# Kernel tuning notes

Hardware: AMD Instinct MI355X
Metric: run time of the kernel (lower is better)

## Reference

```python
import jax, jax.numpy as jnp
import numpy as np


def _up2(x):
    return jnp.repeat(jnp.repeat(x, 2, axis=2), 2, axis=3)


def setup_inputs() -> dict:
    key = jax.random.key(0)
    ks = jax.random.split(key, 6)
    Vps, C, H, W = 32, 128, 64, 64
    return {
        "x1": jax.random.normal(ks[0], (Vps, C, H, W), dtype=jnp.float32),
        "x2": jax.random.normal(ks[1], (Vps, C, H // 2, W // 2), dtype=jnp.float32),
        "x3": jax.random.normal(ks[2], (Vps, C, H // 4, W // 4), dtype=jnp.float32),
        "x4": jax.random.normal(ks[3], (Vps, C, H // 4, W // 4), dtype=jnp.float32),
        "conv_w": jax.random.normal(ks[4], (128, 512), dtype=jnp.float32) * 0.02,
        "conv_b": jnp.zeros((128,), dtype=jnp.float32),
        "gamma": jnp.zeros((1,), dtype=jnp.float32),
        "weight": jnp.ones((128,), dtype=jnp.float32),
        "lin_w": jax.random.normal(ks[5], (1, 128), dtype=jnp.float32) * 0.1,
    }


def reference(x1, x2, x3, x4, conv_w, conv_b, gamma, weight, lin_w):
    # upsample lower pyramid levels to x1 resolution and concat on channels
    x_sm = jnp.concatenate([x1, _up2(x2), _up2(_up2(x3)), _up2(_up2(x4))], axis=1)
    # 1x1 conv: [Vps,512,H,W] x [128,512] -> [Vps,128,H,W]
    x_sm = jnp.einsum('vchw,oc->vohw', x_sm, conv_w) + conv_b[None, :, None, None]
    Vps, C, H, W = x_sm.shape

    # --- batch (viewport) attention ---
    gap = jnp.mean(x_sm, axis=(2, 3))                     # [Vps, C]
    v_q = gap @ lin_w.T                                    # [Vps, 1]
    att = v_q @ v_q.T                                      # [Vps, Vps]
    att_new = jnp.broadcast_to(jnp.max(att, axis=-1, keepdims=True), att.shape)
    vps_mat = jax.nn.softmax(att_new, axis=-1)             # rows constant -> uniform
    v_v = x_sm.reshape(Vps, C * H * W)
    vps_att = (vps_mat @ v_v).reshape(Vps, C, H, W)
    x_sm = vps_att * gamma + x_sm

    # --- channel attention ---
    c_q = jnp.mean(x_sm, axis=(2, 3))                      # [Vps, C]
    att_C = c_q.T @ c_q                                    # [C, C]
    C_mat = jax.nn.softmax(att_C, axis=-1) * weight        # broadcast over last dim
    c_v = x_sm.reshape(C, Vps * H * W)                     # faithful raw reshape as in torch
    C_att = (C_mat @ c_v).reshape(Vps, C, H, W)
    out = C_att + x_sm
    return out.reshape(Vps, C, H * W)
```

## Files before the change

### kernel.cpp

```cpp
#include <hip/hip_runtime.h>

#define V 32
#define CH 128
#define SP 4096

typedef __attribute__((ext_vector_type(8))) short bf16x8;
typedef __attribute__((ext_vector_type(4))) float f32x4;

__device__ __forceinline__ unsigned short bf16rne(float x) {
    union { float f; unsigned u; } v; v.f = x;
    unsigned r = v.u + 0x7fff + ((v.u >> 16) & 1);
    return (unsigned short)(r >> 16);
}

__device__ __forceinline__ int xswz(int s) { return (s & 7) ^ ((s >> 2) & 7); }

__device__ __forceinline__ const float* xsm_row(const float* xsm, int j, int r) {
    return xsm + ((size_t)((j >> 2) * CH + (j & 3) * 32 + r)) * SP;
}

__global__ __launch_bounds__(256) void prep_w(const float* __restrict__ W,
                                              unsigned short* __restrict__ Wpad)
{
    int row = blockIdx.x;
    int j = threadIdx.x;
    if (j < 136) {
        int sigma = row >> 7, o = row & 127;
        float v = (j < 128) ? W[o * 512 + sigma * 128 + j] : 0.f;
        Wpad[row * 136 + j] = bf16rne(v);
    }
}

__global__ __launch_bounds__(256) void conv_lo(
    const float* __restrict__ xa, const float* __restrict__ xb,
    const unsigned short* __restrict__ WA, const unsigned short* __restrict__ WB,
    int spatial, int nph, float* __restrict__ outbuf)
{
    __shared__ __align__(16) unsigned short Wl[128 * 136];
    __shared__ __align__(16) unsigned short Xl[64 * 128];
    const int v = blockIdx.y, sc = blockIdx.x, tid = threadIdx.x;
    const int lane = tid & 63, w = tid >> 6;
    const int l15 = lane & 15, quad = lane >> 4;
    const int o0 = (w >> 1) * 64, s0 = (w & 1) * 32;
    const int sq = tid & 15, cp0 = tid >> 4;

    f32x4 acc[4][2];
#pragma unroll
    for (int it = 0; it < 4; ++it)
#pragma unroll
        for (int st = 0; st < 2; ++st) acc[it][st] = (f32x4){0.f, 0.f, 0.f, 0.f};

#pragma unroll 1
    for (int ph = 0; ph < nph; ++ph) {
        if (ph) __syncthreads();
        const float* xp = ph ? xb : xa;
        const unsigned short* wp = ph ? WB : WA;
        {
            const float4* wsrc = (const float4*)wp;
            float4* wdst = (float4*)Wl;
            for (int idx = tid; idx < 2176; idx += 256) wdst[idx] = wsrc[idx];
        }
        const float* xbase = xp + (size_t)v * CH * spatial + sc * 64;
#pragma unroll
        for (int rep = 0; rep < 4; ++rep) {
            int c = (cp0 + rep * 16) * 2;
            const float* r0 = xbase + (size_t)c * spatial + sq * 4;
            float4 va = *(const float4*)r0;
            float4 vb = *(const float4*)(r0 + spatial);
            float a4[4] = {va.x, va.y, va.z, va.w};
            float b4[4] = {vb.x, vb.y, vb.z, vb.w};
#pragma unroll
            for (int i = 0; i < 4; ++i) {
                int s = sq * 4 + i;
                ushort2 pk; pk.x = bf16rne(a4[i]); pk.y = bf16rne(b4[i]);
                *(ushort2*)&Xl[s * 128 + (((c >> 3) ^ xswz(s)) * 8) + (c & 7)] = pk;
            }
        }
        __syncthreads();
#pragma unroll
        for (int ks = 0; ks < 4; ++ks) {
            int kb = ks * 4 + quad;
            bf16x8 af[4], bfr[2];
#pragma unroll
            for (int it = 0; it < 4; ++it)
                af[it] = *(const bf16x8*)&Wl[(o0 + it * 16 + l15) * 136 + ks * 32 + quad * 8];
#pragma unroll
            for (int st = 0; st < 2; ++st) {
                int s = s0 + st * 16 + l15;
                bfr[st] = *(const bf16x8*)&Xl[s * 128 + ((kb ^ xswz(s)) * 8)];
            }
#pragma unroll
            for (int it = 0; it < 4; ++it)
#pragma unroll
                for (int st = 0; st < 2; ++st)
                    acc[it][st] = __builtin_amdgcn_mfma_f32_16x16x32_bf16(
                        af[it], bfr[st], acc[it][st], 0, 0, 0);
        }
    }
#pragma unroll
    for (int it = 0; it < 4; ++it)
#pragma unroll
        for (int reg = 0; reg < 4; ++reg) {
            int o = o0 + it * 16 + quad * 4 + reg;
            float* orow = outbuf + ((size_t)(v * CH + o)) * spatial + sc * 64;
#pragma unroll
            for (int st = 0; st < 2; ++st) {
                int s_l = s0 + st * 16 + l15;
                orow[s_l] = acc[it][st][reg];
            }
        }
}

__global__ __launch_bounds__(256) void conv_full(
    const float* __restrict__ x1, const unsigned short* __restrict__ W0,
    const float* __restrict__ bias, const float* __restrict__ conv2,
    const float* __restrict__ conv34, float* __restrict__ xsm,
    float* __restrict__ gap)
{
    __shared__ __align__(16) unsigned short Wl[128 * 136];
    __shared__ __align__(16) unsigned short Xl[64 * 128];
    __shared__ float gscr[4][64];
    const int v = blockIdx.y, sc = blockIdx.x, tid = threadIdx.x;
    const int lane = tid & 63, w = tid >> 6;
    const int l15 = lane & 15, quad = lane >> 4;
    const int o0 = (w >> 1) * 64, s0 = (w & 1) * 32;
    const int sq = tid & 15, cp0 = tid >> 4;

    f32x4 acc[4][2];
#pragma unroll
    for (int it = 0; it < 4; ++it)
#pragma unroll
        for (int st = 0; st < 2; ++st) acc[it][st] = (f32x4){0.f, 0.f, 0.f, 0.f};

    {
        const float4* wsrc = (const float4*)W0;
        float4* wdst = (float4*)Wl;
        for (int idx = tid; idx < 2176; idx += 256) wdst[idx] = wsrc[idx];
    }
    const float* xbase = x1 + (size_t)v * CH * SP + sc * 64;
#pragma unroll
    for (int rep = 0; rep < 4; ++rep) {
        int c = (cp0 + rep * 16) * 2;
        const float* r0 = xbase + (size_t)c * SP + sq * 4;
        float4 va = *(const float4*)r0;
        float4 vb = *(const float4*)(r0 + SP);
        float a4[4] = {va.x, va.y, va.z, va.w};
        float b4[4] = {vb.x, vb.y, vb.z, vb.w};
#pragma unroll
        for (int i = 0; i < 4; ++i) {
            int s = sq * 4 + i;
            ushort2 pk; pk.x = bf16rne(a4[i]); pk.y = bf16rne(b4[i]);
            *(ushort2*)&Xl[s * 128 + (((c >> 3) ^ xswz(s)) * 8) + (c & 7)] = pk;
        }
    }
    __syncthreads();
#pragma unroll
    for (int ks = 0; ks < 4; ++ks) {
        int kb = ks * 4 + quad;
        bf16x8 af[4], bfr[2];
#pragma unroll
        for (int it = 0; it < 4; ++it)
            af[it] = *(const bf16x8*)&Wl[(o0 + it * 16 + l15) * 136 + ks * 32 + quad * 8];
#pragma unroll
        for (int st = 0; st < 2; ++st) {
            int s = s0 + st * 16 + l15;
            bfr[st] = *(const bf16x8*)&Xl[s * 128 + ((kb ^ xswz(s)) * 8)];
        }
#pragma unroll
        for (int it = 0; it < 4; ++it)
#pragma unroll
            for (int st = 0; st < 2; ++st)
                acc[it][st] = __builtin_amdgcn_mfma_f32_16x16x32_bf16(
                    af[it], bfr[st], acc[it][st], 0, 0, 0);
    }

    const float* c2row = conv2 + (size_t)v * CH * 1024 + (sc >> 1) * 32;
    const float* c34row = conv34 + (size_t)v * CH * 256 + (sc >> 2) * 16;
    float gs[16];
#pragma unroll
    for (int it = 0; it < 4; ++it)
#pragma unroll
        for (int reg = 0; reg < 4; ++reg) {
            int o = o0 + it * 16 + quad * 4 + reg;
            float b = bias[o];
            float* orow = xsm + ((size_t)(v * CH + o)) * SP + sc * 64;
            const float* c2p = c2row + (size_t)o * 1024;
            const float* c34p = c34row + (size_t)o * 256;
            float lsum = 0.f;
#pragma unroll
            for (int st = 0; st < 2; ++st) {
                int s_l = s0 + st * 16 + l15;
                float val = acc[it][st][reg] + b + c2p[s_l >> 1] + c34p[s_l >> 2];
                orow[s_l] = val;
                lsum += val;
            }
            gs[it * 4 + reg] = lsum;
        }
#pragma unroll
    for (int m = 1; m < 16; m <<= 1)
#pragma unroll
        for (int k = 0; k < 16; ++k) gs[k] += __shfl_xor(gs[k], m, 64);
    if (l15 == 0) {
#pragma unroll
        for (int it = 0; it < 4; ++it)
#pragma unroll
            for (int reg = 0; reg < 4; ++reg)
                gscr[w][it * 16 + quad * 4 + reg] = gs[it * 4 + reg];
    }
    __syncthreads();
    if (tid < 128) {
        int o = tid, b2 = (o >> 6) * 2;
        atomicAdd(&gap[v * CH + o], gscr[b2][o & 63] + gscr[b2 + 1][o & 63]);
    }
}

__global__ __launch_bounds__(128) void build_G(
    const float* __restrict__ gap, const float* __restrict__ gammap,
    const float* __restrict__ weight, unsigned short* __restrict__ GsPad)
{
    __shared__ float cq[32][128];
    __shared__ float red[128];
    const int i = blockIdx.x, j = threadIdx.x;
    const float g = gammap[0];

    float gb = 0.f;
    for (int v = 0; v < 32; ++v) gb += gap[v * CH + j];
    gb = gb * (1.f / 32.f) * (1.f / 4096.f) * g;
    for (int v = 0; v < 32; ++v) cq[v][j] = gap[v * CH + j] * (1.f / 4096.f) + gb;
    __syncthreads();

    float a = 0.f;
    for (int v = 0; v < 32; ++v) a += cq[v][i] * cq[v][j];

    red[j] = a; __syncthreads();
    float m = -1e30f;
    for (int t = 0; t < 128; ++t) m = fmaxf(m, red[t]);
    __syncthreads();
    float e = __expf(a - m);
    red[j] = e; __syncthreads();
    float ssum = 0.f;
    for (int t = 0; t < 128; ++t) ssum += red[t];
    float cm = e / ssum * weight[j] + ((i == j) ? 1.f : 0.f);
    __syncthreads();
    red[j] = cm; __syncthreads();
    float rs = 0.f;
    for (int t = (j & 3); t < 128; t += 4) rs += red[t];
    float gfull = cm + g * (1.f / 32.f) * rs;
    GsPad[i * 136 + j] = bf16rne(gfull - ((i == j) ? 1.f : 0.f));
}

__global__ __launch_bounds__(256) void apply_G(
    float* __restrict__ xsm, const unsigned short* __restrict__ GsPad)
{
    __shared__ __align__(16) unsigned short Gl[128 * 136];
    __shared__ __align__(16) unsigned short Xl[64 * 128];
    const int r = blockIdx.y, sc = blockIdx.x, tid = threadIdx.x;
    const int lane = tid & 63, w = tid >> 6;
    const int l15 = lane & 15, quad = lane >> 4;
    const int i0 = (w >> 1) * 64, s0 = (w & 1) * 32;
    const int sq = tid & 15, cp0 = tid >> 4;

    f32x4 acc[4][2];
#pragma unroll
    for (int it = 0; it < 4; ++it)
#pragma unroll
        for (int st = 0; st < 2; ++st) acc[it][st] = (f32x4){0.f, 0.f, 0.f, 0.f};

    {
        const float4* gsrc = (const float4*)GsPad;
        float4* gdst = (float4*)Gl;
        for (int idx = tid; idx < 2176; idx += 256) gdst[idx] = gsrc[idx];
    }
#pragma unroll
    for (int rep = 0; rep < 4; ++rep) {
        int c = (cp0 + rep * 16) * 2;
        const float* r0 = xsm_row(xsm, c, r) + sc * 64 + sq * 4;
        const float* r1 = xsm_row(xsm, c + 1, r) + sc * 64 + sq * 4;
        float4 va = *(const float4*)r0;
        float4 vb = *(const float4*)r1;
        float a4[4] = {va.x, va.y, va.z, va.w};
        float b4[4] = {vb.x, vb.y, vb.z, vb.w};
#pragma unroll
        for (int i = 0; i < 4; ++i) {
            int s = sq * 4 + i;
            ushort2 pk; pk.x = bf16rne(a4[i]); pk.y = bf16rne(b4[i]);
            *(ushort2*)&Xl[s * 128 + (((c >> 3) ^ xswz(s)) * 8) + (c & 7)] = pk;
        }
    }
    __syncthreads();
#pragma unroll
    for (int ks = 0; ks < 4; ++ks) {
        int kb = ks * 4 + quad;
        bf16x8 af[4], bfr[2];
#pragma unroll
        for (int it = 0; it < 4; ++it)
            af[it] = *(const bf16x8*)&Gl[(i0 + it * 16 + l15) * 136 + ks * 32 + quad * 8];
#pragma unroll
        for (int st = 0; st < 2; ++st) {
            int s = s0 + st * 16 + l15;
            bfr[st] = *(const bf16x8*)&Xl[s * 128 + ((kb ^ xswz(s)) * 8)];
        }
#pragma unroll
        for (int it = 0; it < 4; ++it)
#pragma unroll
            for (int st = 0; st < 2; ++st)
                acc[it][st] = __builtin_amdgcn_mfma_f32_16x16x32_bf16(
                    af[it], bfr[st], acc[it][st], 0, 0, 0);
    }
#pragma unroll
    for (int it = 0; it < 4; ++it)
#pragma unroll
        for (int reg = 0; reg < 4; ++reg) {
            int i = i0 + it * 16 + quad * 4 + reg;
            float* rowp = (float*)xsm_row(xsm, i, r) + sc * 64;
#pragma unroll
            for (int st = 0; st < 2; ++st) {
                int s_l = s0 + st * 16 + l15;
                rowp[s_l] = rowp[s_l] + acc[it][st][reg];
            }
        }
}

extern "C" void kernel_launch(void* const* d_in, const int* in_sizes, int n_in,
                              void* d_out, int out_size, void* d_ws, size_t ws_size,
                              hipStream_t stream)
{
    const float* x1     = (const float*)d_in[0];
    const float* x2     = (const float*)d_in[1];
    const float* x3     = (const float*)d_in[2];
    const float* x4     = (const float*)d_in[3];
    const float* conv_w = (const float*)d_in[4];
    const float* conv_b = (const float*)d_in[5];
    const float* gamma  = (const float*)d_in[6];
    const float* weight = (const float*)d_in[7];

    float* out = (float*)d_out;
    float* ws  = (float*)d_ws;

    float* conv2  = ws;
    float* conv34 = ws + (size_t)4194304;
    float* gap    = ws + (size_t)5242880;
    unsigned short* Wpad  = (unsigned short*)(ws + (size_t)5246976);
    unsigned short* GsPad = (unsigned short*)(ws + (size_t)5281792);

    hipMemsetAsync(gap, 0, 4096 * sizeof(float), stream);

    prep_w<<<512, 256, 0, stream>>>(conv_w, Wpad);
    conv_lo<<<dim3(16, 32), 256, 0, stream>>>(x2, x2, Wpad + 1 * 128 * 136,
                                              Wpad + 1 * 128 * 136, 1024, 1, conv2);
    conv_lo<<<dim3(4, 32), 256, 0, stream>>>(x3, x4, Wpad + 2 * 128 * 136,
                                             Wpad + 3 * 128 * 136, 256, 2, conv34);
    conv_full<<<dim3(64, 32), 256, 0, stream>>>(x1, Wpad, conv_b, conv2, conv34, out, gap);
    build_G<<<128, 128, 0, stream>>>(gap, gamma, weight, GsPad);
    apply_G<<<dim3(64, 32), 256, 0, stream>>>(out, GsPad);
}
```

Measured before the change: 214.7 us.

## Fuse low-resolution convs into full conv via upsampled K-chunks

Removes the two conv_lo kernels and their intermediate buffers. conv_full now upsamples x2, x3 and x4 into shared memory, does the full K=512 reduction as four 128-wide MFMA chunks, and reads weights straight from global memory instead of staging them in LDS. apply_G likewise reads G directly from global memory. This saves kernel launches and the workspace round-trip, but conv_full does four times the MFMA work per block on upsampled data the old code computed once at low resolution, and weight reads now go uncached through global/L2.

Result: slower. 263.5 us (+22.7%).

```diff
diff --git a/kernel.cpp b/kernel.cpp
--- a/kernel.cpp
+++ b/kernel.cpp
@@ -19,112 +19,27 @@
     return xsm + ((size_t)((j >> 2) * CH + (j & 3) * 32 + r)) * SP;
 }
 
-__global__ __launch_bounds__(256) void prep_w(const float* __restrict__ W,
+__global__ __launch_bounds__(128) void prep_w(const float* __restrict__ W,
                                               unsigned short* __restrict__ Wpad)
 {
     int row = blockIdx.x;
     int j = threadIdx.x;
-    if (j < 136) {
-        int sigma = row >> 7, o = row & 127;
-        float v = (j < 128) ? W[o * 512 + sigma * 128 + j] : 0.f;
-        Wpad[row * 136 + j] = bf16rne(v);
-    }
-}
-
-__global__ __launch_bounds__(256) void conv_lo(
-    const float* __restrict__ xa, const float* __restrict__ xb,
-    const unsigned short* __restrict__ WA, const unsigned short* __restrict__ WB,
-    int spatial, int nph, float* __restrict__ outbuf)
-{
-    __shared__ __align__(16) unsigned short Wl[128 * 136];
-    __shared__ __align__(16) unsigned short Xl[64 * 128];
-    const int v = blockIdx.y, sc = blockIdx.x, tid = threadIdx.x;
-    const int lane = tid & 63, w = tid >> 6;
-    const int l15 = lane & 15, quad = lane >> 4;
-    const int o0 = (w >> 1) * 64, s0 = (w & 1) * 32;
-    const int sq = tid & 15, cp0 = tid >> 4;
-
-    f32x4 acc[4][2];
-#pragma unroll
-    for (int it = 0; it < 4; ++it)
-#pragma unroll
-        for (int st = 0; st < 2; ++st) acc[it][st] = (f32x4){0.f, 0.f, 0.f, 0.f};
-
-#pragma unroll 1
-    for (int ph = 0; ph < nph; ++ph) {
-        if (ph) __syncthreads();
-        const float* xp = ph ? xb : xa;
-        const unsigned short* wp = ph ? WB : WA;
-        {
-            const float4* wsrc = (const float4*)wp;
-            float4* wdst = (float4*)Wl;
-            for (int idx = tid; idx < 2176; idx += 256) wdst[idx] = wsrc[idx];
-        }
-        const float* xbase = xp + (size_t)v * CH * spatial + sc * 64;
-#pragma unroll
-        for (int rep = 0; rep < 4; ++rep) {
-            int c = (cp0 + rep * 16) * 2;
-            const float* r0 = xbase + (size_t)c * spatial + sq * 4;
-            float4 va = *(const float4*)r0;
-            float4 vb = *(const float4*)(r0 + spatial);
-            float a4[4] = {va.x, va.y, va.z, va.w};
-            float b4[4] = {vb.x, vb.y, vb.z, vb.w};
-#pragma unroll
-            for (int i = 0; i < 4; ++i) {
-                int s = sq * 4 + i;
-                ushort2 pk; pk.x = bf16rne(a4[i]); pk.y = bf16rne(b4[i]);
-                *(ushort2*)&Xl[s * 128 + (((c >> 3) ^ xswz(s)) * 8) + (c & 7)] = pk;
-            }
-        }
-        __syncthreads();
-#pragma unroll
-        for (int ks = 0; ks < 4; ++ks) {
-            int kb = ks * 4 + quad;
-            bf16x8 af[4], bfr[2];
-#pragma unroll
-            for (int it = 0; it < 4; ++it)
-                af[it] = *(const bf16x8*)&Wl[(o0 + it * 16 + l15) * 136 + ks * 32 + quad * 8];
-#pragma unroll
-            for (int st = 0; st < 2; ++st) {
-                int s = s0 + st * 16 + l15;
-                bfr[st] = *(const bf16x8*)&Xl[s * 128 + ((kb ^ xswz(s)) * 8)];
-            }
-#pragma unroll
-            for (int it = 0; it < 4; ++it)
-#pragma unroll
-                for (int st = 0; st < 2; ++st)
-                    acc[it][st] = __builtin_amdgcn_mfma_f32_16x16x32_bf16(
-                        af[it], bfr[st], acc[it][st], 0, 0, 0);
-        }
-    }
-#pragma unroll
-    for (int it = 0; it < 4; ++it)
-#pragma unroll
-        for (int reg = 0; reg < 4; ++reg) {
-            int o = o0 + it * 16 + quad * 4 + reg;
-            float* orow = outbuf + ((size_t)(v * CH + o)) * spatial + sc * 64;
-#pragma unroll
-            for (int st = 0; st < 2; ++st) {
-                int s_l = s0 + st * 16 + l15;
-                orow[s_l] = acc[it][st][reg];
-            }
-        }
+    int sigma = row >> 7, o = row & 127;
+    Wpad[row * 128 + j] = bf16rne(W[o * 512 + sigma * 128 + j]);
 }
 
 __global__ __launch_bounds__(256) void conv_full(
-    const float* __restrict__ x1, const unsigned short* __restrict__ W0,
-    const float* __restrict__ bias, const float* __restrict__ conv2,
-    const float* __restrict__ conv34, float* __restrict__ xsm,
-    float* __restrict__ gap)
-{
-    __shared__ __align__(16) unsigned short Wl[128 * 136];
+    const float* __restrict__ x1, const float* __restrict__ x2,
+    const float* __restrict__ x3, const float* __restrict__ x4,
+    const unsigned short* __restrict__ Wpad, const float* __restrict__ bias,
+    float* __restrict__ xsm, float* __restrict__ gap)
+{
     __shared__ __align__(16) unsigned short Xl[64 * 128];
     __shared__ float gscr[4][64];
     const int v = blockIdx.y, sc = blockIdx.x, tid = threadIdx.x;
     const int lane = tid & 63, w = tid >> 6;
     const int l15 = lane & 15, quad = lane >> 4;
     const int o0 = (w >> 1) * 64, s0 = (w & 1) * 32;
-    const int sq = tid & 15, cp0 = tid >> 4;
 
     f32x4 acc[4][2];
 #pragma unroll
@@ -132,50 +47,99 @@
 #pragma unroll
         for (int st = 0; st < 2; ++st) acc[it][st] = (f32x4){0.f, 0.f, 0.f, 0.f};
 
+    auto mfma_chunk = [&](const unsigned short* __restrict__ Wsl) {
+#pragma unroll
+        for (int ks = 0; ks < 4; ++ks) {
+            int kb = ks * 4 + quad;
+            bf16x8 af[4], bfr[2];
+#pragma unroll
+            for (int it = 0; it < 4; ++it)
+                af[it] = *(const bf16x8*)&Wsl[(o0 + it * 16 + l15) * 128 + ks * 32 + quad * 8];
+#pragma unroll
+            for (int st = 0; st < 2; ++st) {
+                int s = s0 + st * 16 + l15;
+                bfr[st] = *(const bf16x8*)&Xl[s * 128 + ((kb ^ xswz(s)) * 8)];
+            }
+#pragma unroll
+            for (int it = 0; it < 4; ++it)
+#pragma unroll
+                for (int st = 0; st < 2; ++st)
+                    acc[it][st] = __builtin_amdgcn_mfma_f32_16x16x32_bf16(
+                        af[it], bfr[st], acc[it][st], 0, 0, 0);
+        }
+    };
+
     {
-        const float4* wsrc = (const float4*)W0;
-        float4* wdst = (float4*)Wl;
-        for (int idx = tid; idx < 2176; idx += 256) wdst[idx] = wsrc[idx];
-    }
-    const float* xbase = x1 + (size_t)v * CH * SP + sc * 64;
-#pragma unroll
-    for (int rep = 0; rep < 4; ++rep) {
-        int c = (cp0 + rep * 16) * 2;
-        const float* r0 = xbase + (size_t)c * SP + sq * 4;
-        float4 va = *(const float4*)r0;
-        float4 vb = *(const float4*)(r0 + SP);
-        float a4[4] = {va.x, va.y, va.z, va.w};
-        float b4[4] = {vb.x, vb.y, vb.z, vb.w};
+        const int sq = tid & 15, cp0 = tid >> 4;
+        const float* xbase = x1 + (size_t)v * CH * SP + sc * 64;
+#pragma unroll
+        for (int rep = 0; rep < 4; ++rep) {
+            int c = (cp0 + rep * 16) * 2;
+            const float* r0 = xbase + (size_t)c * SP + sq * 4;
+            float4 va = *(const float4*)r0;
+            float4 vb = *(const float4*)(r0 + SP);
+            float a4[4] = {va.x, va.y, va.z, va.w};
+            float b4[4] = {vb.x, vb.y, vb.z, vb.w};
+#pragma unroll
+            for (int i = 0; i < 4; ++i) {
+                int s = sq * 4 + i;
+                ushort2 pk; pk.x = bf16rne(a4[i]); pk.y = bf16rne(b4[i]);
+                *(ushort2*)&Xl[s * 128 + (((c >> 3) ^ xswz(s)) * 8) + (c & 7)] = pk;
+            }
+        }
+    }
+    __syncthreads();
+    mfma_chunk(Wpad);
+    __syncthreads();
+
+    {
+        const int sqq = tid & 3, c = (tid >> 2) * 2;
+        const float* b2 = x2 + (size_t)(v * CH + c) * 1024 + (sc >> 1) * 32 + sqq * 8;
+        float4 a0 = *(const float4*)b2;
+        float4 a1 = *(const float4*)(b2 + 4);
+        float4 b0 = *(const float4*)(b2 + 1024);
+        float4 b1 = *(const float4*)(b2 + 1028);
+        float av[8] = {a0.x, a0.y, a0.z, a0.w, a1.x, a1.y, a1.z, a1.w};
+        float bv[8] = {b0.x, b0.y, b0.z, b0.w, b1.x, b1.y, b1.z, b1.w};
+#pragma unroll
+        for (int i = 0; i < 8; ++i) {
+            ushort2 pk; pk.x = bf16rne(av[i]); pk.y = bf16rne(bv[i]);
+            int w2 = sqq * 8 + i;
+#pragma unroll
+            for (int d = 0; d < 2; ++d) {
+                int s = w2 * 2 + d;
+                *(ushort2*)&Xl[s * 128 + (((c >> 3) ^ xswz(s)) * 8) + (c & 7)] = pk;
+            }
+        }
+    }
+    __syncthreads();
+    mfma_chunk(Wpad + 1 * 128 * 128);
+    __syncthreads();
+
+#pragma unroll 1
+    for (int ph = 0; ph < 2; ++ph) {
+        const float* xp = ph ? x4 : x3;
+        const int sqq = tid & 3, c = (tid >> 2) * 2;
+        const float* b3 = xp + (size_t)(v * CH + c) * 256 + (sc >> 2) * 16 + sqq * 4;
+        float4 a = *(const float4*)b3;
+        float4 b = *(const float4*)(b3 + 256);
+        float av[4] = {a.x, a.y, a.z, a.w};
+        float bv[4] = {b.x, b.y, b.z, b.w};
 #pragma unroll
         for (int i = 0; i < 4; ++i) {
-            int s = sq * 4 + i;
-            ushort2 pk; pk.x = bf16rne(a4[i]); pk.y = bf16rne(b4[i]);
-            *(ushort2*)&Xl[s * 128 + (((c >> 3) ^ xswz(s)) * 8) + (c & 7)] = pk;
-        }
-    }
-    __syncthreads();
-#pragma unroll
-    for (int ks = 0; ks < 4; ++ks) {
-        int kb = ks * 4 + quad;
-        bf16x8 af[4], bfr[2];
-#pragma unroll
-        for (int it = 0; it < 4; ++it)
-            af[it] = *(const bf16x8*)&Wl[(o0 + it * 16 + l15) * 136 + ks * 32 + quad * 8];
-#pragma unroll
-        for (int st = 0; st < 2; ++st) {
-            int s = s0 + st * 16 + l15;
-            bfr[st] = *(const bf16x8*)&Xl[s * 128 + ((kb ^ xswz(s)) * 8)];
-        }
-#pragma unroll
-        for (int it = 0; it < 4; ++it)
-#pragma unroll
-            for (int st = 0; st < 2; ++st)
-                acc[it][st] = __builtin_amdgcn_mfma_f32_16x16x32_bf16(
-                    af[it], bfr[st], acc[it][st], 0, 0, 0);
-    }
-
-    const float* c2row = conv2 + (size_t)v * CH * 1024 + (sc >> 1) * 32;
-    const float* c34row = conv34 + (size_t)v * CH * 256 + (sc >> 2) * 16;
+            ushort2 pk; pk.x = bf16rne(av[i]); pk.y = bf16rne(bv[i]);
+            int w4 = sqq * 4 + i;
+#pragma unroll
+            for (int d = 0; d < 4; ++d) {
+                int s = w4 * 4 + d;
+                *(ushort2*)&Xl[s * 128 + (((c >> 3) ^ xswz(s)) * 8) + (c & 7)] = pk;
+            }
+        }
+        __syncthreads();
+        mfma_chunk(Wpad + (2 + ph) * 128 * 128);
+        __syncthreads();
+    }
+
     float gs[16];
 #pragma unroll
     for (int it = 0; it < 4; ++it)
@@ -184,13 +148,11 @@
             int o = o0 + it * 16 + quad * 4 + reg;
             float b = bias[o];
             float* orow = xsm + ((size_t)(v * CH + o)) * SP + sc * 64;
-            const float* c2p = c2row + (size_t)o * 1024;
-            const float* c34p = c34row + (size_t)o * 256;
             float lsum = 0.f;
 #pragma unroll
             for (int st = 0; st < 2; ++st) {
                 int s_l = s0 + st * 16 + l15;
-                float val = acc[it][st][reg] + b + c2p[s_l >> 1] + c34p[s_l >> 2];
+                float val = acc[it][st][reg] + b;
                 orow[s_l] = val;
                 lsum += val;
             }
@@ -209,8 +171,8 @@
     }
     __syncthreads();
     if (tid < 128) {
-        int o = tid, b2 = (o >> 6) * 2;
-        atomicAdd(&gap[v * CH + o], gscr[b2][o & 63] + gscr[b2 + 1][o & 63]);
+        int o = tid, b2i = (o >> 6) * 2;
+        atomicAdd(&gap[v * CH + o], gscr[b2i][o & 63] + gscr[b2i + 1][o & 63]);
     }
 }
 
@@ -246,13 +208,12 @@
     float rs = 0.f;
     for (int t = (j & 3); t < 128; t += 4) rs += red[t];
     float gfull = cm + g * (1.f / 32.f) * rs;
-    GsPad[i * 136 + j] = bf16rne(gfull - ((i == j) ? 1.f : 0.f));
+    GsPad[i * 128 + j] = bf16rne(gfull - ((i == j) ? 1.f : 0.f));
 }
 
 __global__ __launch_bounds__(256) void apply_G(
     float* __restrict__ xsm, const unsigned short* __restrict__ GsPad)
 {
-    __shared__ __align__(16) unsigned short Gl[128 * 136];
     __shared__ __align__(16) unsigned short Xl[64 * 128];
     const int r = blockIdx.y, sc = blockIdx.x, tid = threadIdx.x;
     const int lane = tid & 63, w = tid >> 6;
@@ -266,11 +227,6 @@
 #pragma unroll
         for (int st = 0; st < 2; ++st) acc[it][st] = (f32x4){0.f, 0.f, 0.f, 0.f};
 
-    {
-        const float4* gsrc = (const float4*)GsPad;
-        float4* gdst = (float4*)Gl;
-        for (int idx = tid; idx < 2176; idx += 256) gdst[idx] = gsrc[idx];
-    }
 #pragma unroll
     for (int rep = 0; rep < 4; ++rep) {
         int c = (cp0 + rep * 16) * 2;
@@ -294,7 +250,7 @@
         bf16x8 af[4], bfr[2];
 #pragma unroll
         for (int it = 0; it < 4; ++it)
-            af[it] = *(const bf16x8*)&Gl[(i0 + it * 16 + l15) * 136 + ks * 32 + quad * 8];
+            af[it] = *(const bf16x8*)&GsPad[(i0 + it * 16 + l15) * 128 + ks * 32 + quad * 8];
 #pragma unroll
         for (int st = 0; st < 2; ++st) {
             int s = s0 + st * 16 + l15;
@@ -337,20 +293,14 @@
     float* out = (float*)d_out;
     float* ws  = (float*)d_ws;
 
-    float* conv2  = ws;
-    float* conv34 = ws + (size_t)4194304;
-    float* gap    = ws + (size_t)5242880;
-    unsigned short* Wpad  = (unsigned short*)(ws + (size_t)5246976);
-    unsigned short* GsPad = (unsigned short*)(ws + (size_t)5281792);
+    float* gap = ws;
+    unsigned short* Wpad  = (unsigned short*)(ws + 4096);
+    unsigned short* GsPad = Wpad + 4 * 128 * 128;
 
     hipMemsetAsync(gap, 0, 4096 * sizeof(float), stream);
 
-    prep_w<<<512, 256, 0, stream>>>(conv_w, Wpad);
-    conv_lo<<<dim3(16, 32), 256, 0, stream>>>(x2, x2, Wpad + 1 * 128 * 136,
-                                              Wpad + 1 * 128 * 136, 1024, 1, conv2);
-    conv_lo<<<dim3(4, 32), 256, 0, stream>>>(x3, x4, Wpad + 2 * 128 * 136,
-                                             Wpad + 3 * 128 * 136, 256, 2, conv34);
-    conv_full<<<dim3(64, 32), 256, 0, stream>>>(x1, Wpad, conv_b, conv2, conv34, out, gap);
+    prep_w<<<512, 128, 0, stream>>>(conv_w, Wpad);
+    conv_full<<<dim3(64, 32), 256, 0, stream>>>(x1, x2, x3, x4, Wpad, conv_b, out, gap);
     build_G<<<128, 128, 0, stream>>>(gap, gamma, weight, GsPad);
     apply_G<<<dim3(64, 32), 256, 0, stream>>>(out, GsPad);
 }
```
